# Kernel optimization log

Hardware: AMD Instinct MI355X
Metric: run time of the kernel (lower is better)

## Reference

```python
import jax, jax.numpy as jnp
import numpy as np
import math

D_INPUT = 1024
D_Q = 1024
D_K = 1024
D_V = 1024
D_MODEL = 1024
B, S = 4, 2048


def setup_inputs() -> dict:
    key = jax.random.key(0)
    ks = jax.random.split(key, 9)
    sc = 0.02
    return {
        "x": jax.random.normal(ks[0], (B, S, D_INPUT), dtype=jnp.float32),
        "wq": jax.random.normal(ks[1], (D_INPUT, D_Q), dtype=jnp.float32) * sc,
        "bq": jnp.zeros((D_Q,), dtype=jnp.float32),
        "wk": jax.random.normal(ks[2], (D_INPUT, D_K), dtype=jnp.float32) * sc,
        "bk": jnp.zeros((D_K,), dtype=jnp.float32),
        "wv": jax.random.normal(ks[3], (D_INPUT, D_V), dtype=jnp.float32) * sc,
        "bv": jnp.zeros((D_V,), dtype=jnp.float32),
        "wp": jax.random.normal(ks[4], (D_V, D_MODEL), dtype=jnp.float32) * sc,
        "bp": jnp.zeros((D_MODEL,), dtype=jnp.float32),
    }


def reference(x, wq, bq, wk, bk, wv, bv, wp, bp):
    scale = math.sqrt(D_K)  # NOTE: original MULTIPLIES by sqrt(d_k)
    q = x @ wq + bq  # [B,S,Dq]
    k = x @ wk + bk  # [B,S,Dk]
    v = x @ wv + bv  # [B,S,Dv]
    scores = jnp.einsum('bsd,btd->bst', q, k) * scale
    p_attn = jax.nn.softmax(scores, axis=-1)
    # dropout: inference mode (training=False) -> identity
    context = jnp.einsum('bst,btd->bsd', p_attn, v)
    output = context @ wp + bp
    return (output, p_attn)
```

## Files before the change

kernel.cpp:

```cpp
#include <hip/hip_runtime.h>

typedef unsigned short u16;
typedef short bf16x8 __attribute__((ext_vector_type(8)));
typedef float floatx4 __attribute__((ext_vector_type(4)));

static __device__ __forceinline__ u16 f2bf(float f) {
  unsigned int u = __float_as_uint(f);
  unsigned int lsb = (u >> 16) & 1u;
  u += 0x7FFFu + lsb;
  return (u16)(u >> 16);
}
static __device__ __forceinline__ float bf2f(u16 u) {
  return __uint_as_float(((unsigned int)u) << 16);
}

static __device__ __forceinline__ void gl_lds16(const u16* g, u16* l) {
  __builtin_amdgcn_global_load_lds(
      (const __attribute__((address_space(1))) void*)g,
      (__attribute__((address_space(3))) void*)l, 16, 0, 0);
}

template<int WANT_LO>
__global__ __launch_bounds__(256)
void split_transpose_f32(const float* __restrict__ in, u16* __restrict__ hi,
                         u16* __restrict__ lo, int R, int C) {
  __shared__ float t[32][33];
  const int r0 = blockIdx.y * 32, c0 = blockIdx.x * 32;
  const int tid = threadIdx.x;
  const int lr = tid >> 3;
  const int lc = (tid & 7) * 4;
  float4 v = *(const float4*)(in + (size_t)(r0 + lr) * C + c0 + lc);
  t[lr][lc + 0] = v.x; t[lr][lc + 1] = v.y; t[lr][lc + 2] = v.z; t[lr][lc + 3] = v.w;
  __syncthreads();
  u16 ph[4], pl[4];
#pragma unroll
  for (int j = 0; j < 4; j++) {
    float f = t[lc + j][lr];
    ph[j] = f2bf(f);
    if (WANT_LO) pl[j] = f2bf(f - bf2f(ph[j]));
  }
  const size_t o = (size_t)(c0 + lr) * R + r0 + lc;
  *(uint2*)(hi + o) = *(uint2*)ph;
  if (WANT_LO) *(uint2*)(lo + o) = *(uint2*)pl;
}

__global__ __launch_bounds__(256)
void split_f32(const float* __restrict__ in, u16* __restrict__ hi,
               u16* __restrict__ lo) {
  const size_t i4 = ((size_t)blockIdx.x * 256 + threadIdx.x) * 4;
  float4 v = *(const float4*)(in + i4);
  float f[4] = {v.x, v.y, v.z, v.w};
  u16 ph[4], pl[4];
#pragma unroll
  for (int j = 0; j < 4; j++) {
    ph[j] = f2bf(f[j]);
    pl[j] = f2bf(f[j] - bf2f(ph[j]));
  }
  *(uint2*)(hi + i4) = *(uint2*)ph;
  *(uint2*)(lo + i4) = *(uint2*)pl;
}

template<int A_SPLIT, int B_SPLIT, int OUT_MODE, int HAS_BIAS>
__global__ __launch_bounds__(256)
void gemm_mfma(const u16* __restrict__ Ahi, const u16* __restrict__ Alo,
               const u16* __restrict__ Bhi, const u16* __restrict__ Blo,
               const float* __restrict__ bias,
               void* __restrict__ C0, void* __restrict__ C1,
               int M, int N, int K,
               long long aB, long long bB, long long cB, float scale) {
  __shared__ __align__(16) u16 As[(1 + A_SPLIT) * 128 * 32];
  __shared__ __align__(16) u16 Bs[(1 + B_SPLIT) * 128 * 32];

  const int bz = blockIdx.z;
  const u16* A0 = Ahi + (size_t)bz * aB;
  const u16* A1 = A_SPLIT ? (Alo + (size_t)bz * aB) : (const u16*)nullptr;
  const u16* B0 = Bhi + (size_t)bz * bB;
  const u16* B1 = B_SPLIT ? (Blo + (size_t)bz * bB) : (const u16*)nullptr;

  const int m0 = blockIdx.y * 128;
  const int n0 = blockIdx.x * 128;
  const int tid = threadIdx.x;
  const int w = tid >> 6;
  const int L = tid & 63;
  const int rr = L & 15, quad = L >> 4;
  const int wm = (w >> 1) * 64, wn = (w & 1) * 64;

  const int c3 = (L & 3) ^ ((L >> 3) & 3);
  const int srow = w * 32 + (L >> 2);
  u16* stA = &As[w * 1024];
  u16* stB = &Bs[w * 1024];
  const u16* gA0 = A0 + (size_t)(m0 + srow) * K + c3 * 8;
  const u16* gB0 = B0 + (size_t)(n0 + srow) * K + c3 * 8;
  const u16* gA1 = A_SPLIT ? A1 + (size_t)(m0 + srow) * K + c3 * 8 : (const u16*)nullptr;
  const u16* gB1 = B_SPLIT ? B1 + (size_t)(n0 + srow) * K + c3 * 8 : (const u16*)nullptr;

  const int pcb = (quad ^ ((rr >> 1) & 3)) * 8;

  floatx4 acc[4][4] = {};

  for (int k0 = 0; k0 < K; k0 += 32) {
    gl_lds16(gA0 + k0, stA);
    gl_lds16(gA0 + k0 + 16 * (size_t)K, stA + 512);
    gl_lds16(gB0 + k0, stB);
    gl_lds16(gB0 + k0 + 16 * (size_t)K, stB + 512);
    if (A_SPLIT) {
      gl_lds16(gA1 + k0, stA + 4096);
      gl_lds16(gA1 + k0 + 16 * (size_t)K, stA + 4096 + 512);
    }
    if (B_SPLIT) {
      gl_lds16(gB1 + k0, stB + 4096);
      gl_lds16(gB1 + k0 + 16 * (size_t)K, stB + 4096 + 512);
    }
    __syncthreads();

    bf16x8 a0[4], a1[4], b0[4], b1[4];
#pragma unroll
    for (int i = 0; i < 4; i++) {
      const int arow = wm + i * 16 + rr;
      const int brow = wn + i * 16 + rr;
      a0[i] = *(const bf16x8*)&As[arow * 32 + pcb];
      if (A_SPLIT) a1[i] = *(const bf16x8*)&As[4096 + arow * 32 + pcb];
      b0[i] = *(const bf16x8*)&Bs[brow * 32 + pcb];
      if (B_SPLIT) b1[i] = *(const bf16x8*)&Bs[4096 + brow * 32 + pcb];
    }
#pragma unroll
    for (int i = 0; i < 4; i++) {
#pragma unroll
      for (int j = 0; j < 4; j++) {
        acc[i][j] = __builtin_amdgcn_mfma_f32_16x16x32_bf16(a0[i], b0[j], acc[i][j], 0, 0, 0);
        if (A_SPLIT && B_SPLIT) {
          acc[i][j] = __builtin_amdgcn_mfma_f32_16x16x32_bf16(a0[i], b1[j], acc[i][j], 0, 0, 0);
          acc[i][j] = __builtin_amdgcn_mfma_f32_16x16x32_bf16(a1[i], b0[j], acc[i][j], 0, 0, 0);
        }
      }
    }
    __syncthreads();
  }

#pragma unroll
  for (int i = 0; i < 4; i++) {
    const int mbase = m0 + wm + i * 16 + quad * 4;
#pragma unroll
    for (int j = 0; j < 4; j++) {
      const int col = n0 + wn + j * 16 + rr;
      float bvs = 0.f;
      if (HAS_BIAS) bvs = bias[col];
      if (OUT_MODE == 3) {
        u16 pk[4];
#pragma unroll
        for (int ii = 0; ii < 4; ii++) pk[ii] = f2bf(acc[i][j][ii] * scale + bvs);
        const size_t idx = (size_t)(mbase >> 11) * (2048 * 1024) + (size_t)col * 2048 + (mbase & 2047);
        *(uint2*)((u16*)C0 + idx) = *(uint2*)pk;
      } else {
        u16* Cb = (u16*)C0 + (size_t)bz * cB;
        float* Cf = (float*)C0 + (size_t)bz * cB;
        u16* Cl = (OUT_MODE == 1) ? ((u16*)C1 + (size_t)bz * cB) : (u16*)nullptr;
#pragma unroll
        for (int ii = 0; ii < 4; ii++) {
          const float v = acc[i][j][ii] * scale + bvs;
          const size_t idx = (size_t)(mbase + ii) * N + col;
          if (OUT_MODE == 0) {
            Cb[idx] = f2bf(v);
          } else if (OUT_MODE == 1) {
            const u16 h = f2bf(v);
            Cb[idx] = h;
            Cl[idx] = f2bf(v - bf2f(h));
          } else if (OUT_MODE == 2) {
            Cf[idx] = v;
          }
        }
      }
    }
  }
}

__global__ __launch_bounds__(256)
void softmax_rows(float* __restrict__ S, u16* __restrict__ Pb) {
  const int row = blockIdx.x;
  float* s = S + (size_t)row * 2048;
  const int tid = threadIdx.x;
  const int w = tid >> 6;
  __shared__ float redm[4];
  __shared__ float reds[4];

  float v[8];
  float mx = -1e30f;
#pragma unroll
  for (int i = 0; i < 8; i++) {
    v[i] = s[tid + 256 * i];
    mx = fmaxf(mx, v[i]);
  }
#pragma unroll
  for (int o = 32; o > 0; o >>= 1) mx = fmaxf(mx, __shfl_xor(mx, o, 64));
  if ((tid & 63) == 0) redm[w] = mx;
  __syncthreads();
  mx = fmaxf(fmaxf(redm[0], redm[1]), fmaxf(redm[2], redm[3]));

  float sum = 0.f;
#pragma unroll
  for (int i = 0; i < 8; i++) {
    v[i] = __expf(v[i] - mx);
    sum += v[i];
  }
#pragma unroll
  for (int o = 32; o > 0; o >>= 1) sum += __shfl_xor(sum, o, 64);
  if ((tid & 63) == 0) reds[w] = sum;
  __syncthreads();
  sum = reds[0] + reds[1] + reds[2] + reds[3];
  const float rs = 1.0f / sum;
#pragma unroll
  for (int i = 0; i < 8; i++) {
    const float p = v[i] * rs;
    s[tid + 256 * i] = p;
    Pb[(size_t)row * 2048 + tid + 256 * i] = f2bf(p);
  }
}

extern "C" void kernel_launch(void* const* d_in, const int* in_sizes, int n_in,
                              void* d_out, int out_size, void* d_ws, size_t ws_size,
                              hipStream_t stream) {
  const float* x  = (const float*)d_in[0];
  const float* wq = (const float*)d_in[1];
  const float* bq = (const float*)d_in[2];
  const float* wk = (const float*)d_in[3];
  const float* bk = (const float*)d_in[4];
  const float* wv = (const float*)d_in[5];
  const float* bv = (const float*)d_in[6];
  const float* wp = (const float*)d_in[7];
  const float* bp = (const float*)d_in[8];

  const size_t MB = 1024 * 1024;
  char* ws = (char*)d_ws;
  u16* wqThi = (u16*)(ws + 0 * MB);
  u16* wqTlo = (u16*)(ws + 2 * MB);
  u16* wkThi = (u16*)(ws + 4 * MB);
  u16* wkTlo = (u16*)(ws + 6 * MB);
  u16* wvThi = (u16*)(ws + 8 * MB);
  u16* wpThi = (u16*)(ws + 10 * MB);
  u16* xhi   = (u16*)(ws + 12 * MB);
  u16* xlo   = (u16*)(ws + 28 * MB);
  u16* qhi   = (u16*)(ws + 44 * MB);
  u16* qlo   = (u16*)(ws + 60 * MB);
  u16* khi   = (u16*)(ws + 76 * MB);
  u16* klo   = (u16*)(ws + 92 * MB);
  u16* vT    = (u16*)(ws + 108 * MB);
  u16* ctx   = qhi;
  u16* pbf   = khi;

  float* outp = (float*)d_out;
  float* scf  = (float*)d_out + 8388608;

  const dim3 blk(256);

  split_transpose_f32<1><<<dim3(32, 32), blk, 0, stream>>>(wq, wqThi, wqTlo, 1024, 1024);
  split_transpose_f32<1><<<dim3(32, 32), blk, 0, stream>>>(wk, wkThi, wkTlo, 1024, 1024);
  split_transpose_f32<0><<<dim3(32, 32), blk, 0, stream>>>(wv, wvThi, nullptr, 1024, 1024);
  split_transpose_f32<0><<<dim3(32, 32), blk, 0, stream>>>(wp, wpThi, nullptr, 1024, 1024);
  split_f32<<<dim3(8192), blk, 0, stream>>>(x, xhi, xlo);

  gemm_mfma<1, 1, 1, 1><<<dim3(8, 64, 1), blk, 0, stream>>>(
      xhi, xlo, wqThi, wqTlo, bq, qhi, qlo, 8192, 1024, 1024, 0, 0, 0, 1.0f);
  gemm_mfma<1, 1, 1, 1><<<dim3(8, 64, 1), blk, 0, stream>>>(
      xhi, xlo, wkThi, wkTlo, bk, khi, klo, 8192, 1024, 1024, 0, 0, 0, 1.0f);
  gemm_mfma<0, 0, 3, 1><<<dim3(8, 64, 1), blk, 0, stream>>>(
      xhi, nullptr, wvThi, nullptr, bv, vT, nullptr, 8192, 1024, 1024, 0, 0, 0, 1.0f);

  gemm_mfma<1, 1, 2, 0><<<dim3(16, 16, 4), blk, 0, stream>>>(
      qhi, qlo, khi, klo, nullptr, scf, nullptr, 2048, 2048, 1024,
      2048LL * 1024, 2048LL * 1024, 2048LL * 2048, 32.0f);

  softmax_rows<<<dim3(8192), blk, 0, stream>>>(scf, pbf);

  gemm_mfma<0, 0, 0, 0><<<dim3(8, 16, 4), blk, 0, stream>>>(
      pbf, nullptr, vT, nullptr, nullptr, ctx, nullptr, 2048, 1024, 2048,
      2048LL * 2048, 2048LL * 1024, 2048LL * 1024, 1.0f);

  gemm_mfma<0, 0, 2, 1><<<dim3(8, 64, 1), blk, 0, stream>>>(
      ctx, nullptr, wpThi, nullptr, bp, outp, nullptr, 8192, 1024, 1024, 0, 0, 0, 1.0f);
}
```

Before: 535.0 us.

## Fuse Q and K projections into one GEMM and tile two N-blocks per workgroup

Concatenates the transposed Wq/Wk weights and their biases so Q and K are produced by a single GEMM writing an interleaved [8192,2048] buffer. The GEMM now takes explicit leading dimensions and a template T that makes each block process T consecutive 128-wide N tiles, reusing its A row-tile across them. The four weight-transpose launches are merged into one kernel. This cuts launch count and grid size, at the cost of fewer concurrent blocks (the QK^T scores GEMM drops from 1024 to 512 blocks) and some extra strided memory traffic.

Result: faster. 514.8 us (-3.8%).

```diff
diff --git a/kernel.cpp b/kernel.cpp
--- a/kernel.cpp
+++ b/kernel.cpp
@@ -20,16 +20,24 @@
       (__attribute__((address_space(3))) void*)l, 16, 0, 0);
 }
 
-template<int WANT_LO>
-__global__ __launch_bounds__(256)
-void split_transpose_f32(const float* __restrict__ in, u16* __restrict__ hi,
-                         u16* __restrict__ lo, int R, int C) {
+__global__ __launch_bounds__(256)
+void prep_weights(const float* __restrict__ wq, const float* __restrict__ wk,
+                  const float* __restrict__ wv, const float* __restrict__ wp,
+                  u16* __restrict__ qkThi, u16* __restrict__ qkTlo,
+                  u16* __restrict__ wvThi, u16* __restrict__ wpThi) {
   __shared__ float t[32][33];
+  const int z = blockIdx.z;
+  const float* in = (z == 0) ? wq : (z == 1) ? wk : (z == 2) ? wv : wp;
+  u16* hi = (z == 0) ? qkThi : (z == 1) ? (qkThi + 1024 * 1024)
+           : (z == 2) ? wvThi : wpThi;
+  u16* lo = (z == 0) ? qkTlo : (z == 1) ? (qkTlo + 1024 * 1024) : (u16*)nullptr;
+  const int want_lo = (z < 2);
+
   const int r0 = blockIdx.y * 32, c0 = blockIdx.x * 32;
   const int tid = threadIdx.x;
   const int lr = tid >> 3;
   const int lc = (tid & 7) * 4;
-  float4 v = *(const float4*)(in + (size_t)(r0 + lr) * C + c0 + lc);
+  float4 v = *(const float4*)(in + (size_t)(r0 + lr) * 1024 + c0 + lc);
   t[lr][lc + 0] = v.x; t[lr][lc + 1] = v.y; t[lr][lc + 2] = v.z; t[lr][lc + 3] = v.w;
   __syncthreads();
   u16 ph[4], pl[4];
@@ -37,11 +45,18 @@
   for (int j = 0; j < 4; j++) {
     float f = t[lc + j][lr];
     ph[j] = f2bf(f);
-    if (WANT_LO) pl[j] = f2bf(f - bf2f(ph[j]));
-  }
-  const size_t o = (size_t)(c0 + lr) * R + r0 + lc;
+    pl[j] = f2bf(f - bf2f(ph[j]));
+  }
+  const size_t o = (size_t)(c0 + lr) * 1024 + r0 + lc;
   *(uint2*)(hi + o) = *(uint2*)ph;
-  if (WANT_LO) *(uint2*)(lo + o) = *(uint2*)pl;
+  if (want_lo) *(uint2*)(lo + o) = *(uint2*)pl;
+}
+
+__global__ __launch_bounds__(256)
+void concat_bias(const float* __restrict__ bq, const float* __restrict__ bk,
+                 float* __restrict__ out) {
+  const int i = blockIdx.x * 256 + threadIdx.x;
+  out[i] = (i < 1024) ? bq[i] : bk[i - 1024];
 }
 
 __global__ __launch_bounds__(256)
@@ -60,13 +75,13 @@
   *(uint2*)(lo + i4) = *(uint2*)pl;
 }
 
-template<int A_SPLIT, int B_SPLIT, int OUT_MODE, int HAS_BIAS>
+template<int A_SPLIT, int B_SPLIT, int OUT_MODE, int HAS_BIAS, int T>
 __global__ __launch_bounds__(256)
 void gemm_mfma(const u16* __restrict__ Ahi, const u16* __restrict__ Alo,
                const u16* __restrict__ Bhi, const u16* __restrict__ Blo,
                const float* __restrict__ bias,
                void* __restrict__ C0, void* __restrict__ C1,
-               int M, int N, int K,
+               int M, int N, int K, int lda, int ldb, int ldc,
                long long aB, long long bB, long long cB, float scale) {
   __shared__ __align__(16) u16 As[(1 + A_SPLIT) * 128 * 32];
   __shared__ __align__(16) u16 Bs[(1 + B_SPLIT) * 128 * 32];
@@ -78,7 +93,6 @@
   const u16* B1 = B_SPLIT ? (Blo + (size_t)bz * bB) : (const u16*)nullptr;
 
   const int m0 = blockIdx.y * 128;
-  const int n0 = blockIdx.x * 128;
   const int tid = threadIdx.x;
   const int w = tid >> 6;
   const int L = tid & 63;
@@ -89,84 +103,88 @@
   const int srow = w * 32 + (L >> 2);
   u16* stA = &As[w * 1024];
   u16* stB = &Bs[w * 1024];
-  const u16* gA0 = A0 + (size_t)(m0 + srow) * K + c3 * 8;
-  const u16* gB0 = B0 + (size_t)(n0 + srow) * K + c3 * 8;
-  const u16* gA1 = A_SPLIT ? A1 + (size_t)(m0 + srow) * K + c3 * 8 : (const u16*)nullptr;
-  const u16* gB1 = B_SPLIT ? B1 + (size_t)(n0 + srow) * K + c3 * 8 : (const u16*)nullptr;
+  const u16* gA0 = A0 + (size_t)(m0 + srow) * lda + c3 * 8;
+  const u16* gA1 = A_SPLIT ? A1 + (size_t)(m0 + srow) * lda + c3 * 8 : (const u16*)nullptr;
 
   const int pcb = (quad ^ ((rr >> 1) & 3)) * 8;
 
-  floatx4 acc[4][4] = {};
-
-  for (int k0 = 0; k0 < K; k0 += 32) {
-    gl_lds16(gA0 + k0, stA);
-    gl_lds16(gA0 + k0 + 16 * (size_t)K, stA + 512);
-    gl_lds16(gB0 + k0, stB);
-    gl_lds16(gB0 + k0 + 16 * (size_t)K, stB + 512);
-    if (A_SPLIT) {
-      gl_lds16(gA1 + k0, stA + 4096);
-      gl_lds16(gA1 + k0 + 16 * (size_t)K, stA + 4096 + 512);
+  for (int t = 0; t < T; t++) {
+    const int n0 = (blockIdx.x * T + t) * 128;
+    const u16* gB0 = B0 + (size_t)(n0 + srow) * ldb + c3 * 8;
+    const u16* gB1 = B_SPLIT ? B1 + (size_t)(n0 + srow) * ldb + c3 * 8 : (const u16*)nullptr;
+
+    floatx4 acc[4][4] = {};
+
+    for (int k0 = 0; k0 < K; k0 += 32) {
+      gl_lds16(gA0 + k0, stA);
+      gl_lds16(gA0 + k0 + 16 * (size_t)lda, stA + 512);
+      gl_lds16(gB0 + k0, stB);
+      gl_lds16(gB0 + k0 + 16 * (size_t)ldb, stB + 512);
+      if (A_SPLIT) {
+        gl_lds16(gA1 + k0, stA + 4096);
+        gl_lds16(gA1 + k0 + 16 * (size_t)lda, stA + 4096 + 512);
+      }
+      if (B_SPLIT) {
+        gl_lds16(gB1 + k0, stB + 4096);
+        gl_lds16(gB1 + k0 + 16 * (size_t)ldb, stB + 4096 + 512);
+      }
+      __syncthreads();
+
+      bf16x8 a0[4], a1[4], b0[4], b1[4];
+#pragma unroll
+      for (int i = 0; i < 4; i++) {
+        const int arow = wm + i * 16 + rr;
+        const int brow = wn + i * 16 + rr;
+        a0[i] = *(const bf16x8*)&As[arow * 32 + pcb];
+        if (A_SPLIT) a1[i] = *(const bf16x8*)&As[4096 + arow * 32 + pcb];
+        b0[i] = *(const bf16x8*)&Bs[brow * 32 + pcb];
+        if (B_SPLIT) b1[i] = *(const bf16x8*)&Bs[4096 + brow * 32 + pcb];
+      }
+#pragma unroll
+      for (int i = 0; i < 4; i++) {
+#pragma unroll
+        for (int j = 0; j < 4; j++) {
+          acc[i][j] = __builtin_amdgcn_mfma_f32_16x16x32_bf16(a0[i], b0[j], acc[i][j], 0, 0, 0);
+          if (A_SPLIT && B_SPLIT) {
+            acc[i][j] = __builtin_amdgcn_mfma_f32_16x16x32_bf16(a0[i], b1[j], acc[i][j], 0, 0, 0);
+            acc[i][j] = __builtin_amdgcn_mfma_f32_16x16x32_bf16(a1[i], b0[j], acc[i][j], 0, 0, 0);
+          }
+        }
+      }
+      __syncthreads();
     }
-    if (B_SPLIT) {
-      gl_lds16(gB1 + k0, stB + 4096);
-      gl_lds16(gB1 + k0 + 16 * (size_t)K, stB + 4096 + 512);
-    }
-    __syncthreads();
-
-    bf16x8 a0[4], a1[4], b0[4], b1[4];
+
 #pragma unroll
     for (int i = 0; i < 4; i++) {
-      const int arow = wm + i * 16 + rr;
-      const int brow = wn + i * 16 + rr;
-      a0[i] = *(const bf16x8*)&As[arow * 32 + pcb];
-      if (A_SPLIT) a1[i] = *(const bf16x8*)&As[4096 + arow * 32 + pcb];
-      b0[i] = *(const bf16x8*)&Bs[brow * 32 + pcb];
-      if (B_SPLIT) b1[i] = *(const bf16x8*)&Bs[4096 + brow * 32 + pcb];
-    }
-#pragma unroll
-    for (int i = 0; i < 4; i++) {
+      const int mbase = m0 + wm + i * 16 + quad * 4;
 #pragma unroll
       for (int j = 0; j < 4; j++) {
-        acc[i][j] = __builtin_amdgcn_mfma_f32_16x16x32_bf16(a0[i], b0[j], acc[i][j], 0, 0, 0);
-        if (A_SPLIT && B_SPLIT) {
-          acc[i][j] = __builtin_amdgcn_mfma_f32_16x16x32_bf16(a0[i], b1[j], acc[i][j], 0, 0, 0);
-          acc[i][j] = __builtin_amdgcn_mfma_f32_16x16x32_bf16(a1[i], b0[j], acc[i][j], 0, 0, 0);
-        }
-      }
-    }
-    __syncthreads();
-  }
-
-#pragma unroll
-  for (int i = 0; i < 4; i++) {
-    const int mbase = m0 + wm + i * 16 + quad * 4;
-#pragma unroll
-    for (int j = 0; j < 4; j++) {
-      const int col = n0 + wn + j * 16 + rr;
-      float bvs = 0.f;
-      if (HAS_BIAS) bvs = bias[col];
-      if (OUT_MODE == 3) {
-        u16 pk[4];
-#pragma unroll
-        for (int ii = 0; ii < 4; ii++) pk[ii] = f2bf(acc[i][j][ii] * scale + bvs);
-        const size_t idx = (size_t)(mbase >> 11) * (2048 * 1024) + (size_t)col * 2048 + (mbase & 2047);
-        *(uint2*)((u16*)C0 + idx) = *(uint2*)pk;
-      } else {
-        u16* Cb = (u16*)C0 + (size_t)bz * cB;
-        float* Cf = (float*)C0 + (size_t)bz * cB;
-        u16* Cl = (OUT_MODE == 1) ? ((u16*)C1 + (size_t)bz * cB) : (u16*)nullptr;
-#pragma unroll
-        for (int ii = 0; ii < 4; ii++) {
-          const float v = acc[i][j][ii] * scale + bvs;
-          const size_t idx = (size_t)(mbase + ii) * N + col;
-          if (OUT_MODE == 0) {
-            Cb[idx] = f2bf(v);
-          } else if (OUT_MODE == 1) {
-            const u16 h = f2bf(v);
-            Cb[idx] = h;
-            Cl[idx] = f2bf(v - bf2f(h));
-          } else if (OUT_MODE == 2) {
-            Cf[idx] = v;
+        const int col = n0 + wn + j * 16 + rr;
+        float bvs = 0.f;
+        if (HAS_BIAS) bvs = bias[col];
+        if (OUT_MODE == 3) {
+          u16 pk[4];
+#pragma unroll
+          for (int ii = 0; ii < 4; ii++) pk[ii] = f2bf(acc[i][j][ii] * scale + bvs);
+          const size_t idx = (size_t)(mbase >> 11) * (2048 * 1024) + (size_t)col * 2048 + (mbase & 2047);
+          *(uint2*)((u16*)C0 + idx) = *(uint2*)pk;
+        } else {
+          u16* Cb = (u16*)C0 + (size_t)bz * cB;
+          float* Cf = (float*)C0 + (size_t)bz * cB;
+          u16* Cl = (OUT_MODE == 1) ? ((u16*)C1 + (size_t)bz * cB) : (u16*)nullptr;
+#pragma unroll
+          for (int ii = 0; ii < 4; ii++) {
+            const float v = acc[i][j][ii] * scale + bvs;
+            const size_t idx = (size_t)(mbase + ii) * ldc + col;
+            if (OUT_MODE == 0) {
+              Cb[idx] = f2bf(v);
+            } else if (OUT_MODE == 1) {
+              const u16 h = f2bf(v);
+              Cb[idx] = h;
+              Cl[idx] = f2bf(v - bf2f(h));
+            } else if (OUT_MODE == 2) {
+              Cf[idx] = v;
+            }
           }
         }
       }
@@ -231,50 +249,50 @@
 
   const size_t MB = 1024 * 1024;
   char* ws = (char*)d_ws;
-  u16* wqThi = (u16*)(ws + 0 * MB);
-  u16* wqTlo = (u16*)(ws + 2 * MB);
-  u16* wkThi = (u16*)(ws + 4 * MB);
-  u16* wkTlo = (u16*)(ws + 6 * MB);
+  u16* qkThi = (u16*)(ws + 0 * MB);
+  u16* qkTlo = (u16*)(ws + 4 * MB);
   u16* wvThi = (u16*)(ws + 8 * MB);
   u16* wpThi = (u16*)(ws + 10 * MB);
-  u16* xhi   = (u16*)(ws + 12 * MB);
-  u16* xlo   = (u16*)(ws + 28 * MB);
-  u16* qhi   = (u16*)(ws + 44 * MB);
-  u16* qlo   = (u16*)(ws + 60 * MB);
-  u16* khi   = (u16*)(ws + 76 * MB);
-  u16* klo   = (u16*)(ws + 92 * MB);
-  u16* vT    = (u16*)(ws + 108 * MB);
-  u16* ctx   = qhi;
-  u16* pbf   = khi;
+  float* bqk = (float*)(ws + 12 * MB);
+  u16* xhi   = (u16*)(ws + 13 * MB);
+  u16* xlo   = (u16*)(ws + 29 * MB);
+  u16* qkhi  = (u16*)(ws + 45 * MB);
+  u16* qklo  = (u16*)(ws + 77 * MB);
+  u16* vT    = (u16*)(ws + 109 * MB);
+  u16* pbf   = qklo;
+  u16* ctx   = qkhi;
 
   float* outp = (float*)d_out;
   float* scf  = (float*)d_out + 8388608;
 
   const dim3 blk(256);
 
-  split_transpose_f32<1><<<dim3(32, 32), blk, 0, stream>>>(wq, wqThi, wqTlo, 1024, 1024);
-  split_transpose_f32<1><<<dim3(32, 32), blk, 0, stream>>>(wk, wkThi, wkTlo, 1024, 1024);
-  split_transpose_f32<0><<<dim3(32, 32), blk, 0, stream>>>(wv, wvThi, nullptr, 1024, 1024);
-  split_transpose_f32<0><<<dim3(32, 32), blk, 0, stream>>>(wp, wpThi, nullptr, 1024, 1024);
+  prep_weights<<<dim3(32, 32, 4), blk, 0, stream>>>(wq, wk, wv, wp,
+                                                    qkThi, qkTlo, wvThi, wpThi);
+  concat_bias<<<dim3(8), blk, 0, stream>>>(bq, bk, bqk);
   split_f32<<<dim3(8192), blk, 0, stream>>>(x, xhi, xlo);
 
-  gemm_mfma<1, 1, 1, 1><<<dim3(8, 64, 1), blk, 0, stream>>>(
-      xhi, xlo, wqThi, wqTlo, bq, qhi, qlo, 8192, 1024, 1024, 0, 0, 0, 1.0f);
-  gemm_mfma<1, 1, 1, 1><<<dim3(8, 64, 1), blk, 0, stream>>>(
-      xhi, xlo, wkThi, wkTlo, bk, khi, klo, 8192, 1024, 1024, 0, 0, 0, 1.0f);
-  gemm_mfma<0, 0, 3, 1><<<dim3(8, 64, 1), blk, 0, stream>>>(
-      xhi, nullptr, wvThi, nullptr, bv, vT, nullptr, 8192, 1024, 1024, 0, 0, 0, 1.0f);
-
-  gemm_mfma<1, 1, 2, 0><<<dim3(16, 16, 4), blk, 0, stream>>>(
-      qhi, qlo, khi, klo, nullptr, scf, nullptr, 2048, 2048, 1024,
-      2048LL * 1024, 2048LL * 1024, 2048LL * 2048, 32.0f);
+  gemm_mfma<1, 1, 1, 1, 2><<<dim3(8, 64, 1), blk, 0, stream>>>(
+      xhi, xlo, qkThi, qkTlo, bqk, qkhi, qklo,
+      8192, 2048, 1024, 1024, 1024, 2048, 0, 0, 0, 1.0f);
+
+  gemm_mfma<0, 0, 3, 1, 1><<<dim3(8, 64, 1), blk, 0, stream>>>(
+      xhi, nullptr, wvThi, nullptr, bv, vT, nullptr,
+      8192, 1024, 1024, 1024, 1024, 0, 0, 0, 0, 1.0f);
+
+  gemm_mfma<1, 1, 2, 0, 2><<<dim3(8, 16, 4), blk, 0, stream>>>(
+      qkhi, qklo, qkhi + 1024, qklo + 1024, nullptr, scf, nullptr,
+      2048, 2048, 1024, 2048, 2048, 2048,
+      2048LL * 2048, 2048LL * 2048, 2048LL * 2048, 32.0f);
 
   softmax_rows<<<dim3(8192), blk, 0, stream>>>(scf, pbf);
 
-  gemm_mfma<0, 0, 0, 0><<<dim3(8, 16, 4), blk, 0, stream>>>(
-      pbf, nullptr, vT, nullptr, nullptr, ctx, nullptr, 2048, 1024, 2048,
-      2048LL * 2048, 2048LL * 1024, 2048LL * 1024, 1.0f);
-
-  gemm_mfma<0, 0, 2, 1><<<dim3(8, 64, 1), blk, 0, stream>>>(
-      ctx, nullptr, wpThi, nullptr, bp, outp, nullptr, 8192, 1024, 1024, 0, 0, 0, 1.0f);
-}
+  gemm_mfma<0, 0, 0, 0, 1><<<dim3(8, 16, 4), blk, 0, stream>>>(
+      pbf, nullptr, vT, nullptr, nullptr, ctx, nullptr,
+      2048, 1024, 2048, 2048, 2048, 1024,
+      2048LL * 2048, 1024LL * 2048, 2048LL * 1024, 1.0f);
+
+  gemm_mfma<0, 0, 2, 1, 1><<<dim3(8, 64, 1), blk, 0, stream>>>(
+      ctx, nullptr, wpThi, nullptr, bp, outp, nullptr,
+      8192, 1024, 1024, 1024, 1024, 1024, 0, 0, 0, 1.0f);
+}
```
